# Kernel optimization log

Measured on AMD Instinct MI355X. Metric: run time of the kernel, lower is better.

Reference implementation:

```python
import jax, jax.numpy as jnp
import numpy as np

N_NODES = 100000
N_EDGES = 300000
D_IN = 256
D_OUT = 256


def setup_inputs() -> dict:
    key = jax.random.key(0)
    k1, k2, k3 = jax.random.split(key, 3)
    z = jax.random.normal(k1, (N_NODES, D_IN), dtype=jnp.float32)
    edge_index = jax.random.randint(k2, (2, N_EDGES), 0, N_NODES, dtype=jnp.int64)
    # Linear(input_dim, out_dim): weight [out, in], stored transposed for x @ W
    W = jax.random.normal(k3, (D_IN, D_OUT), dtype=jnp.float32) / np.sqrt(D_IN)
    b = jnp.zeros((D_OUT,), dtype=jnp.float32)
    return {"z": z, "edge_index": edge_index, "W": W, "b": b}


def reference(z, edge_index, W, b):
    # h = Linear(z): [N, D_out]
    h = z @ W + b
    # gather endpoint embeddings and take per-edge dot product
    src = h[edge_index[0]]  # [E, D_out]
    dst = h[edge_index[1]]  # [E, D_out]
    value = jnp.sum(src * dst, axis=1)  # [E]
    return jax.nn.sigmoid(value)
```

## Files before the change

kernel.cpp:

```cpp
#include <hip/hip_runtime.h>
#include <hip/hip_bf16.h>
#include <hip/hip_fp16.h>
#include <math.h>


#define D_DIM 256
#define BM 64

typedef __attribute__((ext_vector_type(8))) _Float16 half8;
typedef __attribute__((ext_vector_type(4))) float f32x4;

__device__ half8 g_Wf[8 * 256 * 4];

__global__ __launch_bounds__(256) void pack_w_kernel(const float* __restrict__ W) {
  int t = blockIdx.x * 256 + threadIdx.x;
  int kb = t >> 10;
  int qd = (t >> 8) & 3;
  int n  = t & 255;
  half8 o;
#pragma unroll
  for (int j = 0; j < 8; j++)
    o[j] = (_Float16)W[(size_t)(kb * 32 + qd * 8 + j) * D_DIM + n];
  g_Wf[(kb * 256 + n) * 4 + qd] = o;
}

__device__ inline void stage_b(int kb, char* buf, int wv, int lane) {
  const char* gsrc = (const char*)g_Wf + (size_t)kb * 16384 + wv * 2048;
  char* ldst = buf + wv * 2048;
#pragma unroll
  for (int i = 0; i < 2; i++) {
    __builtin_amdgcn_global_load_lds(
        (const __attribute__((address_space(1))) void*)(gsrc + i * 1024 + lane * 16),
        (__attribute__((address_space(3))) void*)(ldst + i * 1024),
        16, 0, 0);
  }
}

__global__ __launch_bounds__(512) void gemm_mfma_kernel(
    const float* __restrict__ z, const float* __restrict__ b,
    __half* __restrict__ h, int nrows) {
  __shared__ char smem[34816];
  const int tid = threadIdx.x;
  const int lane = tid & 63;
  const int wv = tid >> 6;
  const int mf = wv >> 1;
  const int nh = wv & 1;
  const int fr = lane & 15;
  const int qd = lane >> 4;
  const int row0 = blockIdx.x * BM + mf * 16;

  f32x4 acc[8];
#pragma unroll
  for (int j = 0; j < 8; j++) acc[j] = (f32x4)0.f;

  int ar = row0 + fr;
  ar = ar < nrows ? ar : (nrows - 1);
  const float* zrow = z + (size_t)ar * D_DIM + qd * 8;

  float4 a0 = *(const float4*)(zrow);
  float4 a1 = *(const float4*)(zrow + 4);
  stage_b(0, smem, wv, lane);
  __syncthreads();

#pragma unroll 1
  for (int kb = 0; kb < 8; kb++) {
    char* cur = smem + (kb & 1) * 16384;
    if (kb < 7) stage_b(kb + 1, smem + ((kb + 1) & 1) * 16384, wv, lane);

    half8 af;
    af[0] = (_Float16)a0.x; af[1] = (_Float16)a0.y;
    af[2] = (_Float16)a0.z; af[3] = (_Float16)a0.w;
    af[4] = (_Float16)a1.x; af[5] = (_Float16)a1.y;
    af[6] = (_Float16)a1.z; af[7] = (_Float16)a1.w;
    if (kb < 7) {
      const float* p = zrow + (kb + 1) * 32;
      a0 = *(const float4*)(p);
      a1 = *(const float4*)(p + 4);
    }

    const half8* buf = (const half8*)cur;
#pragma unroll
    for (int fn = 0; fn < 8; fn++) {
      int fi = (nh * 128 + fn * 16 + fr) * 4 + qd;
      half8 bf = buf[fi];
      acc[fn] = __builtin_amdgcn_mfma_f32_16x16x32_f16(af, bf, acc[fn], 0, 0, 0);
    }
    __syncthreads();
  }

  __half* et = (__half*)(smem + wv * 4352);
  float bias[8];
#pragma unroll
  for (int fn = 0; fn < 8; fn++) bias[fn] = b[nh * 128 + fn * 16 + fr];

#pragma unroll
  for (int fn = 0; fn < 8; fn++)
#pragma unroll
    for (int r = 0; r < 4; r++)
      et[(qd * 4 + r) * 136 + fn * 16 + fr] = __float2half(acc[fn][r] + bias[fn]);
#pragma unroll
  for (int p = 0; p < 4; p++) {
    int idx = p * 64 + lane;
    int rr = idx >> 4;
    int cc = idx & 15;
    float4 v = *(const float4*)(et + rr * 136 + cc * 8);
    int row = row0 + rr;
    if (row < nrows)
      *(float4*)(h + (size_t)row * D_DIM + nh * 128 + cc * 8) = v;
  }
}

__global__ __launch_bounds__(256) void edge_dot_kernel(
    const int* __restrict__ ei, const __half* __restrict__ h,
    float* __restrict__ out, int E) {
  int wid = (blockIdx.x * blockDim.x + threadIdx.x) >> 6;
  int lane = threadIdx.x & 63;
  int ebase = wid * 8;
  if (ebase >= E) return;
  const int half = lane >> 5;
  const int off = lane & 31;

  float4 v[8];
#pragma unroll
  for (int q = 0; q < 8; q++) {
    int e = ebase + q;
    e = e < E ? e : (E - 1);
    int node = half ? ei[E + e] : ei[e];
    v[q] = *(const float4*)((const __half*)h + (size_t)node * D_DIM + off * 8);
  }

  float res = 0.f;
#pragma unroll
  for (int q = 0; q < 8; q++) {
    float4 w;
    w.x = __shfl_xor(v[q].x, 32);
    w.y = __shfl_xor(v[q].y, 32);
    w.z = __shfl_xor(v[q].z, 32);
    w.w = __shfl_xor(v[q].w, 32);
    const __half2* a2 = (const __half2*)&v[q];
    const __half2* b2 = (const __half2*)&w;
    float part = 0.f;
#pragma unroll
    for (int j = 0; j < 4; j++) {
      float2 fa = __half22float2(a2[j]);
      float2 fb = __half22float2(b2[j]);
      part += fa.x * fb.x + fa.y * fb.y;
    }
#pragma unroll
    for (int m = 1; m <= 16; m <<= 1) part += __shfl_xor(part, m);
    res = (lane == q) ? part : res;
  }
  if (lane < 8) {
    int e = ebase + lane;
    if (e < E) out[e] = 1.0f / (1.0f + __expf(-res));
  }
}

extern "C" void kernel_launch(void* const* d_in, const int* in_sizes, int n_in,
                              void* d_out, int out_size, void* d_ws, size_t ws_size,
                              hipStream_t stream) {
  const float* z  = (const float*)d_in[0];
  const int*   ei = (const int*)d_in[1];
  const float* W  = (const float*)d_in[2];
  const float* b  = (const float*)d_in[3];
  float* out = (float*)d_out;
  __half* h  = (__half*)d_ws;

  const int nnodes = in_sizes[0] / D_DIM;
  const int E = in_sizes[1] / 2;

  pack_w_kernel<<<32, 256, 0, stream>>>(W);

  dim3 grid_gemm((nnodes + BM - 1) / BM);
  gemm_mfma_kernel<<<grid_gemm, 512, 0, stream>>>(z, b, h, nnodes);

  int waves = (E + 7) / 8;
  dim3 grid_edge(((size_t)waves * 64 + 255) / 256);
  edge_dot_kernel<<<grid_edge, 256, 0, stream>>>(ei, h, out, E);
}
```

Measured before the change: 218.0 us.

## Widen GEMM tile to 128 rows, each wave owning full 256-col output

The GEMM block tile grows from 64 to 128 rows. Each of 8 waves now computes 16 rows across all 256 columns with 16 accumulators, so the 8 k-step double-buffered pipeline becomes two 64KB LDS half-loads of the packed weights. All of a wave's z-row loads are issued up front to raise memory-level parallelism. This halves the number of blocks and the per-block weight reloads per row, at the cost of more registers (16 acc + 16 float4), 64KB of LDS per block limiting occupancy, and no overlap of weight staging with compute.

Result: no change. 220.9 us (+1.3%).

```diff
diff --git a/kernel.cpp b/kernel.cpp
--- a/kernel.cpp
+++ b/kernel.cpp
@@ -5,7 +5,7 @@
 
 
 #define D_DIM 256
-#define BM 64
+#define BM 128
 
 typedef __attribute__((ext_vector_type(8))) _Float16 half8;
 typedef __attribute__((ext_vector_type(4))) float f32x4;
@@ -24,14 +24,14 @@
   g_Wf[(kb * 256 + n) * 4 + qd] = o;
 }
 
-__device__ inline void stage_b(int kb, char* buf, int wv, int lane) {
-  const char* gsrc = (const char*)g_Wf + (size_t)kb * 16384 + wv * 2048;
-  char* ldst = buf + wv * 2048;
+__device__ inline void stage_half(const char* gsrc, char* buf, int wv, int lane) {
+  const char* s = gsrc + wv * 8192;
+  char* d = buf + wv * 8192;
 #pragma unroll
-  for (int i = 0; i < 2; i++) {
+  for (int i = 0; i < 8; i++) {
     __builtin_amdgcn_global_load_lds(
-        (const __attribute__((address_space(1))) void*)(gsrc + i * 1024 + lane * 16),
-        (__attribute__((address_space(3))) void*)(ldst + i * 1024),
+        (const __attribute__((address_space(1))) void*)(s + i * 1024 + lane * 16),
+        (__attribute__((address_space(3))) void*)(d + i * 1024),
         16, 0, 0);
   }
 }
@@ -39,74 +39,85 @@
 __global__ __launch_bounds__(512) void gemm_mfma_kernel(
     const float* __restrict__ z, const float* __restrict__ b,
     __half* __restrict__ h, int nrows) {
-  __shared__ char smem[34816];
+  __shared__ char smem[65536];
   const int tid = threadIdx.x;
   const int lane = tid & 63;
   const int wv = tid >> 6;
-  const int mf = wv >> 1;
-  const int nh = wv & 1;
   const int fr = lane & 15;
   const int qd = lane >> 4;
-  const int row0 = blockIdx.x * BM + mf * 16;
+  const int row0 = blockIdx.x * BM + wv * 16;
 
-  f32x4 acc[8];
+  int r = row0 + fr;
+  r = r < nrows ? r : (nrows - 1);
+  const float* zrow = z + (size_t)r * D_DIM + qd * 8;
+
+  float4 a0[8], a1[8];
 #pragma unroll
-  for (int j = 0; j < 8; j++) acc[j] = (f32x4)0.f;
+  for (int kb = 0; kb < 8; kb++) {
+    const float* p = zrow + kb * 32;
+    a0[kb] = *(const float4*)(p);
+    a1[kb] = *(const float4*)(p + 4);
+  }
 
-  int ar = row0 + fr;
-  ar = ar < nrows ? ar : (nrows - 1);
-  const float* zrow = z + (size_t)ar * D_DIM + qd * 8;
+  f32x4 acc[16];
+#pragma unroll
+  for (int j = 0; j < 16; j++) acc[j] = (f32x4)0.f;
 
-  float4 a0 = *(const float4*)(zrow);
-  float4 a1 = *(const float4*)(zrow + 4);
-  stage_b(0, smem, wv, lane);
+  stage_half((const char*)g_Wf, smem, wv, lane);
+  __syncthreads();
+#pragma unroll
+  for (int s = 0; s < 4; s++) {
+    half8 af;
+    af[0] = (_Float16)a0[s].x; af[1] = (_Float16)a0[s].y;
+    af[2] = (_Float16)a0[s].z; af[3] = (_Float16)a0[s].w;
+    af[4] = (_Float16)a1[s].x; af[5] = (_Float16)a1[s].y;
+    af[6] = (_Float16)a1[s].z; af[7] = (_Float16)a1[s].w;
+#pragma unroll
+    for (int fn = 0; fn < 16; fn++) {
+      half8 bf = *(const half8*)(smem + s * 16384 + fn * 1024 + fr * 64 + qd * 16);
+      acc[fn] = __builtin_amdgcn_mfma_f32_16x16x32_f16(af, bf, acc[fn], 0, 0, 0);
+    }
+  }
   __syncthreads();
 
-#pragma unroll 1
-  for (int kb = 0; kb < 8; kb++) {
-    char* cur = smem + (kb & 1) * 16384;
-    if (kb < 7) stage_b(kb + 1, smem + ((kb + 1) & 1) * 16384, wv, lane);
-
+  stage_half((const char*)g_Wf + 65536, smem, wv, lane);
+  __syncthreads();
+#pragma unroll
+  for (int s = 0; s < 4; s++) {
     half8 af;
-    af[0] = (_Float16)a0.x; af[1] = (_Float16)a0.y;
-    af[2] = (_Float16)a0.z; af[3] = (_Float16)a0.w;
-    af[4] = (_Float16)a1.x; af[5] = (_Float16)a1.y;
-    af[6] = (_Float16)a1.z; af[7] = (_Float16)a1.w;
-    if (kb < 7) {
-      const float* p = zrow + (kb + 1) * 32;
-      a0 = *(const float4*)(p);
-      a1 = *(const float4*)(p + 4);
-    }
-
-    const half8* buf = (const half8*)cur;
+    af[0] = (_Float16)a0[s + 4].x; af[1] = (_Float16)a0[s + 4].y;
+    af[2] = (_Float16)a0[s + 4].z; af[3] = (_Float16)a0[s + 4].w;
+    af[4] = (_Float16)a1[s + 4].x; af[5] = (_Float16)a1[s + 4].y;
+    af[6] = (_Float16)a1[s + 4].z; af[7] = (_Float16)a1[s + 4].w;
 #pragma unroll
-    for (int fn = 0; fn < 8; fn++) {
-      int fi = (nh * 128 + fn * 16 + fr) * 4 + qd;
-      half8 bf = buf[fi];
+    for (int fn = 0; fn < 16; fn++) {
+      half8 bf = *(const half8*)(smem + s * 16384 + fn * 1024 + fr * 64 + qd * 16);
       acc[fn] = __builtin_amdgcn_mfma_f32_16x16x32_f16(af, bf, acc[fn], 0, 0, 0);
     }
-    __syncthreads();
   }
+  __syncthreads();
 
   __half* et = (__half*)(smem + wv * 4352);
-  float bias[8];
 #pragma unroll
-  for (int fn = 0; fn < 8; fn++) bias[fn] = b[nh * 128 + fn * 16 + fr];
-
+  for (int ph = 0; ph < 2; ph++) {
 #pragma unroll
-  for (int fn = 0; fn < 8; fn++)
+    for (int f8 = 0; f8 < 8; f8++) {
+      int fn = ph * 8 + f8;
+      float bias = b[fn * 16 + fr];
 #pragma unroll
-    for (int r = 0; r < 4; r++)
-      et[(qd * 4 + r) * 136 + fn * 16 + fr] = __float2half(acc[fn][r] + bias[fn]);
+      for (int rr = 0; rr < 4; rr++)
+        et[(qd * 4 + rr) * 136 + f8 * 16 + fr] = __float2half(acc[fn][rr] + bias);
+    }
 #pragma unroll
-  for (int p = 0; p < 4; p++) {
-    int idx = p * 64 + lane;
-    int rr = idx >> 4;
-    int cc = idx & 15;
-    float4 v = *(const float4*)(et + rr * 136 + cc * 8);
-    int row = row0 + rr;
-    if (row < nrows)
-      *(float4*)(h + (size_t)row * D_DIM + nh * 128 + cc * 8) = v;
+    for (int p = 0; p < 4; p++) {
+      int idx = p * 64 + lane;
+      int rr = idx >> 4;
+      int cc = idx & 15;
+      float4 v = *(const float4*)(et + rr * 136 + cc * 8);
+      int row = row0 + rr;
+      if (row < nrows)
+        *(float4*)(h + (size_t)row * D_DIM + ph * 128 + cc * 8) = v;
+    }
   }
 }
 
```
